# Kernel optimization log

Hardware: AMD Instinct MI355X
Metric: run time of the kernel (lower is better)

The kernel has to match this reference:

```python
import jax, jax.numpy as jnp
import numpy as np

K_MIN = 30.0
TAU = 1e-06
BETA = 0.9
LAMBDA_MAX = 0.1
LAMBDA_SCALE = 1.0

N, D_OUT, N_MODULES, N_CONTEXTS = 262144, 128, 64, 16


def setup_inputs() -> dict:
    key = jax.random.key(0)
    k1, k2, k3, k4 = jax.random.split(key, 4)
    Y_hat = jax.random.normal(k1, (N, D_OUT), dtype=jnp.float32)
    context_weights = jax.random.uniform(k2, (N, N_CONTEXTS), dtype=jnp.float32)
    M_pinv = jax.random.normal(k3, (N_MODULES, D_OUT), dtype=jnp.float32) * 0.1
    C_prior = jax.random.normal(k4, (N_CONTEXTS, N_MODULES, N_MODULES), dtype=jnp.float32) * 0.1
    # Buffers exactly as registered in __init__
    ema_Sigma = jnp.broadcast_to(jnp.eye(N_MODULES, dtype=jnp.float32), (N_CONTEXTS, N_MODULES, N_MODULES))
    ema_sigma_sq = jnp.ones((N_CONTEXTS, N_MODULES), dtype=jnp.float32)
    ema_initialized = jnp.zeros((N_CONTEXTS,), dtype=bool)
    return {"Y_hat": Y_hat, "context_weights": context_weights, "M_pinv": M_pinv,
            "C_prior": C_prior, "ema_Sigma": ema_Sigma, "ema_sigma_sq": ema_sigma_sq,
            "ema_initialized": ema_initialized}


def reference(Y_hat, context_weights, M_pinv, C_prior, ema_Sigma, ema_sigma_sq, ema_initialized):
    # Z_hat: [N, m]
    Z = Y_hat @ M_pinv.T
    wsum = context_weights.sum(axis=0)            # [T] == eff_n per context
    active = wsum >= K_MIN                        # context skipping, vectorized
    # Weighted mean per context: [T, m]
    mu = (context_weights.T @ Z) / wsum[:, None]
    # Weighted covariance: sum_n w_norm * (z-mu)(z-mu)^T == E_w[zz^T] - mu mu^T
    w_norm = context_weights / wsum[None, :]      # [N, T]
    S = jnp.einsum('nt,nm,nk->tmk', w_norm, Z, Z)  # [T, m, m]
    Sigma = S - mu[:, :, None] * mu[:, None, :]
    # EMA sigma_sq update (no-grad in original -> stop_gradient)
    Sigma_sg = jax.lax.stop_gradient(Sigma)
    diag_init = jnp.diagonal(Sigma_sg, axis1=1, axis2=2)                       # first-call branch
    diag_ema = jnp.diagonal(BETA * ema_Sigma + (1.0 - BETA) * Sigma_sg, axis1=1, axis2=2)
    sigma_sq = jnp.where(ema_initialized[:, None], diag_ema, diag_init)        # [T, m]
    std = jnp.sqrt(sigma_sq + TAU)
    denom = std[:, :, None] * std[:, None, :]
    C_hat = jnp.clip(Sigma / (denom + TAU), -1.0, 1.0)
    loss_t = jnp.sum((C_hat - C_prior) ** 2, axis=(1, 2)) / wsum               # [T]
    n_active = jnp.sum(active)
    total = jnp.sum(jnp.where(active, loss_t, 0.0))
    total = jnp.where(n_active > 0,
                      LAMBDA_MAX * LAMBDA_SCALE * total / jnp.maximum(n_active, 1).astype(total.dtype),
                      jnp.zeros((), total.dtype))
    return total
```

## Files before the change

### kernel.cpp

```cpp
#include <hip/hip_runtime.h>
#include <stdint.h>

#define N_ROWS 262144
#define D_OUTC 128
#define M_MOD  64
#define T_CTX  16

#define ZB_OFF   ((size_t)0)
#define ZB_BYTES ((size_t)M_MOD * N_ROWS * 2)
#define WT_OFF   (ZB_OFF + ZB_BYTES)
#define WT_BYTES ((size_t)T_CTX * N_ROWS * 2)
#define SS_OFF   (WT_OFF + WT_BYTES)
#define SS_BYTES ((size_t)T_CTX * M_MOD * M_MOD * 4)
#define B_OFF    (SS_OFF + SS_BYTES)
#define B_BYTES  ((size_t)T_CTX * M_MOD * 4)
#define WSUM_OFF (B_OFF + B_BYTES)
#define WSUM_BYTES ((size_t)64)
#define LT_OFF   (WSUM_OFF + WSUM_BYTES)
#define LT_BYTES ((size_t)64)
#define PSS_OFF  (LT_OFF + LT_BYTES)
#define PSS_BYTES ((size_t)256 * T_CTX * M_MOD * M_MOD * 2)
#define NEED_BIG (PSS_OFF + PSS_BYTES)

typedef __attribute__((ext_vector_type(4))) float f32x4;
typedef __attribute__((ext_vector_type(8))) _Float16 f16x8;
typedef __attribute__((ext_vector_type(2))) _Float16 h2;

union FR { uint4 u; f16x8 v; h2 h[4]; };

__device__ __forceinline__ float bf2f(unsigned short u) {
  return __uint_as_float(((unsigned int)u) << 16);
}
__device__ __forceinline__ unsigned short f2bf(float f) {
  unsigned int x = __float_as_uint(f);
  return (unsigned short)((x + 0x7fffu + ((x >> 16) & 1u)) >> 16);
}
__device__ __forceinline__ h2 cvt_pkrtz(float a, float b) {
  return __builtin_bit_cast(h2, __builtin_amdgcn_cvt_pkrtz(a, b));
}
#if __has_builtin(__builtin_amdgcn_fdot2)
__device__ __forceinline__ float fdot2f(h2 a, h2 b, float c) {
  return __builtin_amdgcn_fdot2(a, b, c, false);
}
#else
__device__ __forceinline__ float fdot2f(h2 a, h2 b, float c) {
  return c + (float)a[0] * (float)b[0] + (float)a[1] * (float)b[1];
}
#endif

#define WAITVM(N) asm volatile("s_waitcnt vmcnt(" #N ")" ::: "memory")
#define SBAR() do { __builtin_amdgcn_s_barrier(); __builtin_amdgcn_sched_barrier(0); } while (0)

__global__ __launch_bounds__(256, 3) void zk_kernel(
    const float* __restrict__ Y, const float* __restrict__ Mp,
    const float* __restrict__ W,
    _Float16* __restrict__ Zbt, _Float16* __restrict__ Wt)
{
  __shared__ __align__(16) float    Yl[64 * 128];
  __shared__ __align__(16) _Float16 Mpl[64 * 128];
  __shared__ float Wf[16][65];
  const int tid  = threadIdx.x;
  const int l    = tid & 63;
  const int wv   = tid >> 6;
  const int g    = l >> 4;
  const int col  = l & 15;
  const int n0   = blockIdx.x * 64;

#pragma unroll
  for (int k = 0; k < 8; ++k) {
    const int pr  = wv * 8 + k;
    const int row = pr * 2 + (l >> 5);
    const int q   = l & 31;
    const int b   = (q & ~7) | ((q & 7) ^ (row & 7));
    const float* src = Y + ((size_t)(n0 + row)) * D_OUTC + b * 4;
    __builtin_amdgcn_global_load_lds((const unsigned int*)src,
        (unsigned int*)((char*)&Yl[0] + pr * 1024), 16, 0, 0);
  }
  {
    const int m  = tid >> 2;
    const int dq = tid & 3;
#pragma unroll
    for (int i = 0; i < 4; ++i) {
      const int s = dq * 4 + i;
      const float* mp = Mp + (size_t)m * D_OUTC + s * 8;
      float4 a = *(const float4*)mp;
      float4 b = *(const float4*)(mp + 4);
      FR o;
      o.h[0] = cvt_pkrtz(a.x, a.y); o.h[1] = cvt_pkrtz(a.z, a.w);
      o.h[2] = cvt_pkrtz(b.x, b.y); o.h[3] = cvt_pkrtz(b.z, b.w);
      const int ss = (s & ~7) | ((s & 7) ^ (m & 7));
      *(uint4*)((char*)&Mpl[0] + m * 256 + ss * 16) = o.u;
    }
  }
  {
    const int r  = tid >> 2;
    const int c0 = (tid & 3) * 4;
    float4 wv4 = *(const float4*)(W + (size_t)(n0 + r) * T_CTX + c0);
    Wf[c0 + 0][r] = wv4.x; Wf[c0 + 1][r] = wv4.y;
    Wf[c0 + 2][r] = wv4.z; Wf[c0 + 3][r] = wv4.w;
  }
  __syncthreads();
  {
    const int t = tid >> 4, ni = tid & 15;
    h2 h0 = cvt_pkrtz(Wf[t][4 * ni], Wf[t][4 * ni + 1]);
    h2 h1 = cvt_pkrtz(Wf[t][4 * ni + 2], Wf[t][4 * ni + 3]);
    uint2 pk = {__builtin_bit_cast(unsigned int, h0), __builtin_bit_cast(unsigned int, h1)};
    *(uint2*)(Wt + (size_t)t * N_ROWS + n0 + 4 * ni) = pk;
  }
  f32x4 acc[4];
#pragma unroll
  for (int qi = 0; qi < 4; ++qi) acc[qi] = (f32x4){0.f, 0.f, 0.f, 0.f};
  const int nrow = wv * 16 + col;
#pragma unroll
  for (int ks = 0; ks < 4; ++ks) {
    const char* yb = (const char*)&Yl[0] + nrow * 512 + ks * 128;
    uint4 y0 = *(const uint4*)(yb + 16 * ((2 * g) ^ (nrow & 7)));
    uint4 y1 = *(const uint4*)(yb + 16 * ((2 * g + 1) ^ (nrow & 7)));
    const float* f0 = (const float*)&y0;
    const float* f1 = (const float*)&y1;
    FR B;
    B.h[0] = cvt_pkrtz(f0[0], f0[1]); B.h[1] = cvt_pkrtz(f0[2], f0[3]);
    B.h[2] = cvt_pkrtz(f1[0], f1[1]); B.h[3] = cvt_pkrtz(f1[2], f1[3]);
#pragma unroll
    for (int qi = 0; qi < 4; ++qi) {
      const int m = qi * 16 + col;
      const int s = ks * 4 + g;
      FR A;
      A.u = *(const uint4*)((char*)&Mpl[0] + m * 256 + 16 * ((s & ~7) | ((s & 7) ^ (m & 7))));
      acc[qi] = __builtin_amdgcn_mfma_f32_16x16x32_f16(A.v, B.v, acc[qi], 0, 0, 0);
    }
  }
#pragma unroll
  for (int qi = 0; qi < 4; ++qi)
#pragma unroll
    for (int i = 0; i < 4; ++i)
      Zbt[(size_t)(qi * 16 + g * 4 + i) * N_ROWS + n0 + wv * 16 + col] =
          (_Float16)acc[qi][i];
}

#define SS_NS 256
template <bool PARTIAL>
__global__ __launch_bounds__(256, 3) void ss_kernel(
    const _Float16* __restrict__ Zbt, const _Float16* __restrict__ Wt,
    float* __restrict__ SS, float* __restrict__ Bm,
    unsigned short* __restrict__ Pss)
{
  __shared__ __align__(16) _Float16 Zl[3][64 * 128];
  __shared__ __align__(16) _Float16 Wl[3][4 * 128];
  const int tid = threadIdx.x;
  const int l   = tid & 63;
  const int wv  = tid >> 6;
  const int g   = l >> 4;
  const int col = l & 15;
  const int swz = (col & 7) << 4;
  const int ns  = blockIdx.x & (SS_NS - 1);
  const int cg  = blockIdx.x >> 8;
  const int ctx = cg * 4 + wv;
  const int n0b = ns * 1024;
  const int zr    = l >> 4;
  const int zslot = l & 15;

  f32x4 acc[4][4];
  f32x4 accB[4];
#pragma unroll
  for (int a = 0; a < 4; ++a) {
    accB[a] = (f32x4){0.f, 0.f, 0.f, 0.f};
#pragma unroll
    for (int b = 0; b < 4; ++b) acc[a][b] = (f32x4){0.f, 0.f, 0.f, 0.f};
  }
  FR ones;
#pragma unroll
  for (int j = 0; j < 4; ++j) ones.h[j] = (h2){(_Float16)1.f, (_Float16)1.f};

  auto stage = [&](int c, int buf) {
    const int n0 = n0b + c * 128;
#pragma unroll
    for (int i = 0; i < 4; ++i) {
      const int zm = 16 * wv + 4 * i + zr;
      const _Float16* src = Zbt + (size_t)zm * N_ROWS + n0 + 8 * (zslot ^ (zm & 7));
      __builtin_amdgcn_global_load_lds((const unsigned int*)src,
          (unsigned int*)((char*)&Zl[buf][0] + (16 * wv + 4 * i) * 256), 16, 0, 0);
    }
    const _Float16* wsrc = Wt + (size_t)(cg * 4 + zr) * N_ROWS + n0 + 8 * zslot;
    __builtin_amdgcn_global_load_lds((const unsigned int*)wsrc,
        (unsigned int*)((char*)&Wl[buf][0]), 16, 0, 0);
  };

  stage(0, 0);
  stage(1, 1);
  WAITVM(5);
  SBAR();

#pragma unroll
  for (int c = 0; c < 8; ++c) {
    const int buf = c % 3;
    if (c < 6) stage(c + 2, (c + 2) % 3);
    const char* zb = (const char*)&Zl[buf][0];
    const char* wb = (const char*)&Wl[buf][0];
#pragma unroll
    for (int s = 0; s < 4; ++s) {
      FR wfr;
      wfr.u = *(const uint4*)(wb + wv * 256 + s * 64 + g * 16);
      const int cby = ((s * 64 + g * 16) ^ swz);
      FR fr[4];
#pragma unroll
      for (int qi = 0; qi < 4; ++qi)
        fr[qi].u = *(const uint4*)(zb + (qi * 16 + col) * 256 + cby);
      __builtin_amdgcn_s_setprio(1);
#pragma unroll
      for (int qi = 0; qi < 4; ++qi) {
        FR A;
#pragma unroll
        for (int j = 0; j < 4; ++j) A.h[j] = fr[qi].h[j] * wfr.h[j];
        accB[qi] = __builtin_amdgcn_mfma_f32_16x16x32_f16(A.v, ones.v, accB[qi], 0, 0, 0);
#pragma unroll
        for (int ki = 0; ki < 4; ++ki)
          acc[qi][ki] = __builtin_amdgcn_mfma_f32_16x16x32_f16(A.v, fr[ki].v, acc[qi][ki], 0, 0, 0);
      }
      __builtin_amdgcn_s_setprio(0);
    }
    if (c < 6)      { WAITVM(5); SBAR(); }
    else if (c < 7) { WAITVM(0); SBAR(); }
  }

  if (col == 0) {
#pragma unroll
    for (int qi = 0; qi < 4; ++qi)
#pragma unroll
      for (int i = 0; i < 4; ++i)
        atomicAdd(&Bm[ctx * 64 + qi * 16 + g * 4 + i], accB[qi][i]);
  }
  if (PARTIAL) {
    unsigned short* P = Pss + ((size_t)ns * 16 + ctx) * 4096;
#pragma unroll
    for (int qi = 0; qi < 4; ++qi)
#pragma unroll
      for (int ki = 0; ki < 4; ++ki)
#pragma unroll
        for (int i = 0; i < 4; ++i)
          P[(qi * 16 + g * 4 + i) * 64 + ki * 16 + col] = f2bf(acc[qi][ki][i]);
  } else {
#pragma unroll
    for (int qi = 0; qi < 4; ++qi)
#pragma unroll
      for (int ki = 0; ki < 4; ++ki)
#pragma unroll
        for (int i = 0; i < 4; ++i)
          atomicAdd(&SS[(size_t)ctx * 4096 + (qi * 16 + g * 4 + i) * 64 + ki * 16 + col],
                    acc[qi][ki][i]);
  }
}

__global__ __launch_bounds__(256) void wsk_kernel(const _Float16* __restrict__ Wt,
                                                  float* __restrict__ wsum)
{
  const int tid = threadIdx.x;
  const int t = blockIdx.x >> 2, q = blockIdx.x & 3;
  const uint4* base = (const uint4*)(Wt + (size_t)t * N_ROWS + q * 65536);
  const h2 one2 = {(_Float16)1.f, (_Float16)1.f};
  float s = 0.f;
  for (int i = tid; i < 8192; i += 256) {
    uint4 v = base[i];
    const h2* h = (const h2*)&v;
#pragma unroll
    for (int j = 0; j < 4; ++j) s = fdot2f(h[j], one2, s);
  }
  s += __shfl_xor(s, 1);  s += __shfl_xor(s, 2);
  s += __shfl_xor(s, 4);  s += __shfl_xor(s, 8);
  s += __shfl_xor(s, 16); s += __shfl_xor(s, 32);
  __shared__ float red[4];
  if ((tid & 63) == 0) red[tid >> 6] = s;
  __syncthreads();
  if (tid == 0) atomicAdd(&wsum[t], red[0] + red[1] + red[2] + red[3]);
}

__global__ __launch_bounds__(256) void ssred_kernel(
    const unsigned short* __restrict__ Pss, float* __restrict__ SS)
{
  const int e = blockIdx.x * 256 + threadIdx.x;
  float s = 0.f;
#pragma unroll 8
  for (int b = 0; b < 256; ++b)
    s += bf2f(Pss[(size_t)b * 65536 + e]);
  SS[e] = s;
}

__global__ __launch_bounds__(64) void fin1_kernel(
    const float* __restrict__ SS, const float* __restrict__ Bm,
    const float* __restrict__ wsum, const float* __restrict__ Cp,
    const float* __restrict__ emaS, const unsigned char* __restrict__ inited,
    float* __restrict__ LT)
{
  const int t = blockIdx.x, m = threadIdx.x;
  __shared__ float muL[64], stdL[64];
  const float ws  = wsum[t];
  const float inv = 1.0f / ws;
  const float mu  = Bm[t * 64 + m] * inv;
  {
    float Smm = SS[(size_t)t * 4096 + m * 65] * inv - mu * mu;
    float de  = 0.9f * emaS[(size_t)t * 4096 + m * 65] + 0.1f * Smm;
    float sq  = inited[t] ? de : Smm;
    muL[m]  = mu;
    stdL[m] = sqrtf(sq + 1e-6f);
  }
  __syncthreads();
  const float sm = stdL[m];
  const float* SSr = SS + (size_t)t * 4096 + m * 64;
  const float* Cpr = Cp + (size_t)t * 4096 + m * 64;
  float acc = 0.f;
#pragma unroll
  for (int k = 0; k < 64; ++k) {
    float Sig = SSr[k] * inv - mu * muL[k];
    float den = sm * stdL[k] + 1e-6f;
    float ch  = fminf(1.f, fmaxf(-1.f, Sig / den));
    float d   = ch - Cpr[k];
    acc = fmaf(d, d, acc);
  }
#pragma unroll
  for (int o = 1; o < 64; o <<= 1) acc += __shfl_xor(acc, o);
  if (m == 0) LT[t] = acc * inv;
}

__global__ __launch_bounds__(64) void fin2_kernel(
    const float* __restrict__ LT, const float* __restrict__ wsum,
    float* __restrict__ out)
{
  const int l = threadIdx.x;
  float lt = 0.f, act = 0.f;
  if (l < 16) {
    float ws = wsum[l];
    if (ws >= 30.0f) { act = 1.f; lt = LT[l]; }
  }
#pragma unroll
  for (int o = 1; o < 16; o <<= 1) {
    lt  += __shfl_xor(lt, o);
    act += __shfl_xor(act, o);
  }
  if (l == 0) out[0] = (act > 0.f) ? (0.1f * 1.0f * lt / act) : 0.f;
}

extern "C" void kernel_launch(void* const* d_in, const int* in_sizes, int n_in,
                              void* d_out, int out_size, void* d_ws, size_t ws_size,
                              hipStream_t stream) {
  (void)in_sizes; (void)n_in; (void)out_size;
  const float* Y    = (const float*)d_in[0];
  const float* W    = (const float*)d_in[1];
  const float* Mp   = (const float*)d_in[2];
  const float* Cp   = (const float*)d_in[3];
  const float* emaS = (const float*)d_in[4];
  const unsigned char* inited = (const unsigned char*)d_in[6];
  float* out = (float*)d_out;
  char* ws = (char*)d_ws;
  _Float16* Zbt = (_Float16*)(ws + ZB_OFF);
  _Float16* Wt  = (_Float16*)(ws + WT_OFF);
  float* SS   = (float*)(ws + SS_OFF);
  float* Bm   = (float*)(ws + B_OFF);
  float* wsum = (float*)(ws + WSUM_OFF);
  float* LT   = (float*)(ws + LT_OFF);
  unsigned short* Pss = (unsigned short*)(ws + PSS_OFF);

  zk_kernel<<<N_ROWS / 64, 256, 0, stream>>>(Y, Mp, W, Zbt, Wt);
  if (ws_size >= NEED_BIG) {
    (void)hipMemsetAsync(ws + B_OFF, 0, B_BYTES + WSUM_BYTES, stream);
    ss_kernel<true><<<4 * SS_NS, 256, 0, stream>>>(Zbt, Wt, SS, Bm, Pss);
    wsk_kernel<<<64, 256, 0, stream>>>(Wt, wsum);
    ssred_kernel<<<256, 256, 0, stream>>>(Pss, SS);
  } else {
    (void)hipMemsetAsync(ws + SS_OFF, 0, SS_BYTES + B_BYTES + WSUM_BYTES, stream);
    ss_kernel<false><<<4 * SS_NS, 256, 0, stream>>>(Zbt, Wt, SS, Bm, Pss);
    wsk_kernel<<<64, 256, 0, stream>>>(Wt, wsum);
  }
  fin1_kernel<<<16, 64, 0, stream>>>(SS, Bm, wsum, Cp, emaS, inited, LT);
  fin2_kernel<<<1, 64, 0, stream>>>(LT, wsum, out);
}
```

Baseline: 150.1 us.

## Widen ss_kernel to 8 contexts per block with 4-stage 64-row Z pipeline

Blocks now have 512 threads, one wave per context for 8 contexts, so each Z tile in shared memory is reused by twice as many contexts and total Z traffic from global memory halves. The pipeline moves to 64-row chunks with four shared-memory buffers and three loads in flight. The whole weight slice for the block is loaded up front. Shared memory per block shrinks, which allows 4 blocks per CU, but the grid is halved to 512 blocks and the larger blocks may lower occupancy per wave.

```diff
diff --git a/kernel.cpp b/kernel.cpp
--- a/kernel.cpp
+++ b/kernel.cpp
@@ -139,26 +139,24 @@
 }
 
 #define SS_NS 256
+#define NCH   16
 template <bool PARTIAL>
-__global__ __launch_bounds__(256, 3) void ss_kernel(
+__global__ __launch_bounds__(512, 4) void ss_kernel(
     const _Float16* __restrict__ Zbt, const _Float16* __restrict__ Wt,
     float* __restrict__ SS, float* __restrict__ Bm,
     unsigned short* __restrict__ Pss)
 {
-  __shared__ __align__(16) _Float16 Zl[3][64 * 128];
-  __shared__ __align__(16) _Float16 Wl[3][4 * 128];
+  __shared__ __align__(16) _Float16 Zl[4][64 * 64];
+  __shared__ __align__(16) _Float16 Wlds[8 * 1024];
   const int tid = threadIdx.x;
   const int l   = tid & 63;
   const int wv  = tid >> 6;
   const int g   = l >> 4;
   const int col = l & 15;
-  const int swz = (col & 7) << 4;
   const int ns  = blockIdx.x & (SS_NS - 1);
   const int cg  = blockIdx.x >> 8;
-  const int ctx = cg * 4 + wv;
+  const int ctx = cg * 8 + wv;
   const int n0b = ns * 1024;
-  const int zr    = l >> 4;
-  const int zslot = l & 15;
 
   f32x4 acc[4][4];
   f32x4 accB[4];
@@ -172,40 +170,39 @@
 #pragma unroll
   for (int j = 0; j < 4; ++j) ones.h[j] = (h2){(_Float16)1.f, (_Float16)1.f};
 
-  auto stage = [&](int c, int buf) {
-    const int n0 = n0b + c * 128;
-#pragma unroll
-    for (int i = 0; i < 4; ++i) {
-      const int zm = 16 * wv + 4 * i + zr;
-      const _Float16* src = Zbt + (size_t)zm * N_ROWS + n0 + 8 * (zslot ^ (zm & 7));
-      __builtin_amdgcn_global_load_lds((const unsigned int*)src,
-          (unsigned int*)((char*)&Zl[buf][0] + (16 * wv + 4 * i) * 256), 16, 0, 0);
-    }
-    const _Float16* wsrc = Wt + (size_t)(cg * 4 + zr) * N_ROWS + n0 + 8 * zslot;
+#pragma unroll
+  for (int k = 0; k < 2; ++k) {
+    const _Float16* wsrc = Wt + (size_t)ctx * N_ROWS + n0b + k * 512 + l * 8;
     __builtin_amdgcn_global_load_lds((const unsigned int*)wsrc,
-        (unsigned int*)((char*)&Wl[buf][0]), 16, 0, 0);
+        (unsigned int*)((char*)&Wlds[0] + wv * 2048 + k * 1024), 16, 0, 0);
+  }
+  const int zrow  = 8 * wv + (l >> 3);
+  const int zslot = l & 7;
+  auto stage = [&](int c) {
+    const int n0 = n0b + c * 64;
+    const _Float16* src = Zbt + (size_t)zrow * N_ROWS + n0 + 8 * (zslot ^ (zrow & 7));
+    __builtin_amdgcn_global_load_lds((const unsigned int*)src,
+        (unsigned int*)((char*)&Zl[c & 3][0] + wv * 1024 + l * 16), 16, 0, 0);
   };
 
-  stage(0, 0);
-  stage(1, 1);
-  WAITVM(5);
+  stage(0); stage(1); stage(2);
+  WAITVM(2);
   SBAR();
 
-#pragma unroll
-  for (int c = 0; c < 8; ++c) {
-    const int buf = c % 3;
-    if (c < 6) stage(c + 2, (c + 2) % 3);
-    const char* zb = (const char*)&Zl[buf][0];
-    const char* wb = (const char*)&Wl[buf][0];
-#pragma unroll
-    for (int s = 0; s < 4; ++s) {
+  for (int c = 0; c < NCH; ++c) {
+    if (c + 3 < NCH) stage(c + 3);
+    const char* zb = (const char*)&Zl[c & 3][0];
+    const char* wb = (const char*)&Wlds[0] + wv * 2048 + c * 128;
+#pragma unroll
+    for (int s = 0; s < 2; ++s) {
       FR wfr;
-      wfr.u = *(const uint4*)(wb + wv * 256 + s * 64 + g * 16);
-      const int cby = ((s * 64 + g * 16) ^ swz);
+      wfr.u = *(const uint4*)(wb + s * 64 + g * 16);
       FR fr[4];
 #pragma unroll
-      for (int qi = 0; qi < 4; ++qi)
-        fr[qi].u = *(const uint4*)(zb + (qi * 16 + col) * 256 + cby);
+      for (int qi = 0; qi < 4; ++qi) {
+        const int r = qi * 16 + col;
+        fr[qi].u = *(const uint4*)(zb + r * 128 + 16 * ((s * 4 + g) ^ (r & 7)));
+      }
       __builtin_amdgcn_s_setprio(1);
 #pragma unroll
       for (int qi = 0; qi < 4; ++qi) {
@@ -219,8 +216,9 @@
       }
       __builtin_amdgcn_s_setprio(0);
     }
-    if (c < 6)      { WAITVM(5); SBAR(); }
-    else if (c < 7) { WAITVM(0); SBAR(); }
+    if (c + 3 < NCH)      { WAITVM(2); SBAR(); }
+    else if (c == NCH - 3) { WAITVM(1); SBAR(); }
+    else if (c == NCH - 2) { WAITVM(0); SBAR(); }
   }
 
   if (col == 0) {
@@ -362,12 +360,12 @@
   zk_kernel<<<N_ROWS / 64, 256, 0, stream>>>(Y, Mp, W, Zbt, Wt);
   if (ws_size >= NEED_BIG) {
     (void)hipMemsetAsync(ws + B_OFF, 0, B_BYTES + WSUM_BYTES, stream);
-    ss_kernel<true><<<4 * SS_NS, 256, 0, stream>>>(Zbt, Wt, SS, Bm, Pss);
+    ss_kernel<true><<<2 * SS_NS, 512, 0, stream>>>(Zbt, Wt, SS, Bm, Pss);
     wsk_kernel<<<64, 256, 0, stream>>>(Wt, wsum);
     ssred_kernel<<<256, 256, 0, stream>>>(Pss, SS);
   } else {
     (void)hipMemsetAsync(ws + SS_OFF, 0, SS_BYTES + B_BYTES + WSUM_BYTES, stream);
-    ss_kernel<false><<<4 * SS_NS, 256, 0, stream>>>(Zbt, Wt, SS, Bm, Pss);
+    ss_kernel<false><<<2 * SS_NS, 512, 0, stream>>>(Zbt, Wt, SS, Bm, Pss);
     wsk_kernel<<<64, 256, 0, stream>>>(Wt, wsum);
   }
   fin1_kernel<<<16, 64, 0, stream>>>(SS, Bm, wsum, Cp, emaS, inited, LT);
```

After: 138.2 us. 1.09x faster.
